# Optimization experiments

Measured on AMD Instinct MI355X. Metric: run time of the kernel, lower is better.

The kernel has to match this reference:

```python
import jax, jax.numpy as jnp
import numpy as np

B, S, D = 2, 2048, 1024
H, DH, DM = 16, 64, 4096
EPS = 1e-5
IGNORE = -100000.0


def setup_inputs() -> dict:
    key = jax.random.key(0)
    ks = jax.random.split(key, 14)
    s = 0.02
    return {
        "x": jax.random.normal(ks[0], (B, S, D), jnp.float32),
        "W_Q": jax.random.normal(ks[1], (H, DH, D), jnp.float32) * s,
        "W_K": jax.random.normal(ks[2], (H, DH, D), jnp.float32) * s,
        "W_V": jax.random.normal(ks[3], (H, DH, D), jnp.float32) * s,
        "W_O": jax.random.normal(ks[4], (H, D, DH), jnp.float32) * s,
        "b_Q": jax.random.normal(ks[5], (H, DH), jnp.float32) * s,
        "b_K": jax.random.normal(ks[6], (H, DH), jnp.float32) * s,
        "b_V": jax.random.normal(ks[7], (H, DH), jnp.float32) * s,
        "b_O": jax.random.normal(ks[8], (D,), jnp.float32) * s,
        "W_in": jax.random.normal(ks[9], (DM, D), jnp.float32) * s,
        "b_in": jax.random.normal(ks[10], (DM,), jnp.float32) * s,
        "W_out": jax.random.normal(ks[11], (D, DM), jnp.float32) * s,
        "b_out": jax.random.normal(ks[12], (D,), jnp.float32) * s,
    }


def ln_pre(x):
    x = x - jnp.mean(x, axis=-1, keepdims=True)
    scale = jnp.sqrt(jnp.mean(x * x, axis=-1, keepdims=True) + EPS)
    return x / scale


def gelu_new(x):
    c = np.sqrt(2.0 / np.pi).astype(np.float32)
    return 0.5 * x * (1.0 + jnp.tanh(c * (x + 0.044715 * x ** 3)))


def reference(x, W_Q, W_K, W_V, W_O, b_Q, b_K, b_V, b_O, W_in, b_in, W_out, b_out):
    resid_pre = x
    xn = ln_pre(resid_pre)
    # q,k,v: [B, S, H, DH]
    q = jnp.einsum('ihm,bpm->bpih', W_Q, xn) + b_Q
    k = jnp.einsum('ihm,bpm->bpih', W_K, xn) + b_K
    v = jnp.einsum('ihm,bpm->bpih', W_V, xn) + b_V
    attn_scale = np.sqrt(DH).astype(np.float32)
    # scores: [B, H, Sq, Sk]  (einsum 'bpih,bqih->bipq')
    scores = jnp.einsum('bpih,bqih->bipq', q, k) / attn_scale
    mask = jnp.tril(jnp.ones((S, S), bool))
    scores = jnp.where(mask, scores, IGNORE)
    attn = jax.nn.softmax(scores, axis=-1)
    # z: [B, Sq, H, DH]
    z = jnp.einsum('bpih,biqp->bqih', v, attn)
    attn_out = jnp.einsum('idh,bqih->bqd', W_O, z) + b_O
    resid_mid = resid_pre + attn_out
    m = ln_pre(resid_mid)
    pre = jnp.einsum('md,bpd->bpm', W_in, m) + b_in
    post = gelu_new(pre)
    mlp_out = jnp.einsum('dm,bpm->bpd', W_out, post) + b_out
    return resid_mid + mlp_out
```

## Files before the change

### kernel.cpp

```cpp
#include <hip/hip_runtime.h>

typedef unsigned short u16;
typedef __attribute__((ext_vector_type(8))) short short8;
typedef __attribute__((ext_vector_type(4))) unsigned short ushort4v;
typedef __attribute__((ext_vector_type(4))) float float4v;

__device__ __forceinline__ float bf2f(u16 u) {
  union { unsigned int i; float f; } c; c.i = ((unsigned int)u) << 16; return c.f;
}
__device__ __forceinline__ u16 f2bf(float f) {
  union { float f; unsigned int i; } c; c.f = f;
  unsigned int u = c.i;
  return (u16)((u + 0x7fffu + ((u >> 16) & 1u)) >> 16);
}
__device__ __forceinline__ unsigned int cvt_pk_bf16(float a, float b) {
  unsigned int r;
  asm("v_cvt_pk_bf16_f32 %0, %1, %2" : "=v"(r) : "v"(a), "v"(b));
  return r;
}
__device__ __forceinline__ float gelu_new(float x) {
  const float k1 = 2.30218776f;
  const float k3 = 0.10294233f;
  float x3 = x * x * x;
  float e = __builtin_amdgcn_exp2f(-(k1 * x + k3 * x3));
  return x / (1.0f + e);
}
__device__ __forceinline__ float ldres(const float* p) { return *p; }
__device__ __forceinline__ float ldres(const u16* p) { return bf2f(*p); }

__device__ __forceinline__ void gload_lds16(const u16* g, u16* l) {
  __builtin_amdgcn_global_load_lds(
      (const __attribute__((address_space(1))) unsigned int*)g,
      (__attribute__((address_space(3))) unsigned int*)l, 16, 0, 0);
}

__global__ void cvt_bf16_multi(const float* __restrict__ s0, const float* __restrict__ s1,
                               const float* __restrict__ s2, const float* __restrict__ s3,
                               const float* __restrict__ s4, u16* __restrict__ d0,
                               u16* __restrict__ d1, u16* __restrict__ d2,
                               u16* __restrict__ d3, u16* __restrict__ d4) {
  int bid = blockIdx.x;
  const float* src; u16* dst; int base;
  if (bid < 512)       { src = s0; dst = d0; base = 0; }
  else if (bid < 1024) { src = s1; dst = d1; base = 512; }
  else if (bid < 1536) { src = s2; dst = d2; base = 1024; }
  else if (bid < 3584) { src = s3; dst = d3; base = 1536; }
  else                 { src = s4; dst = d4; base = 3584; }
  int t = (bid - base) * 256 + threadIdx.x;
  float4v a = *(const float4v*)(src + (size_t)t * 8);
  float4v b = *(const float4v*)(src + (size_t)t * 8 + 4);
  short8 o;
#pragma unroll
  for (int j = 0; j < 4; ++j) o[j] = (short)f2bf(a[j]);
#pragma unroll
  for (int j = 0; j < 4; ++j) o[4 + j] = (short)f2bf(b[j]);
  *(short8*)(dst + (size_t)t * 8) = o;
}

__global__ void prep_wo(const float* __restrict__ WO, u16* __restrict__ Wot) {
  int t = blockIdx.x * 256 + threadIdx.x;
  int i = t >> 13;
  int d = (t >> 3) & 1023;
  int h0 = (t & 7) * 8;
  const float* src = WO + (size_t)i * 65536 + d * 64 + h0;
  float4v a = *(const float4v*)(src);
  float4v b = *(const float4v*)(src + 4);
  short8 o;
#pragma unroll
  for (int j = 0; j < 4; ++j) o[j] = (short)f2bf(a[j]);
#pragma unroll
  for (int j = 0; j < 4; ++j) o[4 + j] = (short)f2bf(b[j]);
  *(short8*)(Wot + (size_t)d * 1024 + i * 64 + h0) = o;
}

__global__ void prep_bqkv(const float* __restrict__ bQ, const float* __restrict__ bK,
                          const float* __restrict__ bV, float* __restrict__ bqkv) {
  int t = blockIdx.x * 256 + threadIdx.x;
  if (t < 3072)
    bqkv[t] = (t < 1024) ? bQ[t] : (t < 2048) ? bK[t - 1024] : bV[t - 2048];
}

__global__ void ln_f32(const float* __restrict__ x, u16* __restrict__ y) {
  __shared__ float red1[4];
  __shared__ float red2[4];
  int token = blockIdx.x;
  int tid = threadIdx.x;
  int w = tid >> 6;
  const float* xr = x + (size_t)token * 1024;
  float4v v = *(const float4v*)(xr + tid * 4);
  float s = v[0] + v[1] + v[2] + v[3];
#pragma unroll
  for (int m = 32; m >= 1; m >>= 1) s += __shfl_xor(s, m);
  if ((tid & 63) == 0) red1[w] = s;
  __syncthreads();
  float mean = (red1[0] + red1[1] + red1[2] + red1[3]) * (1.0f / 1024.0f);
  float ss = 0.0f;
#pragma unroll
  for (int j = 0; j < 4; ++j) { v[j] -= mean; ss += v[j] * v[j]; }
#pragma unroll
  for (int m = 32; m >= 1; m >>= 1) ss += __shfl_xor(ss, m);
  if ((tid & 63) == 0) red2[w] = ss;
  __syncthreads();
  float ms = (red2[0] + red2[1] + red2[2] + red2[3]) * (1.0f / 1024.0f);
  float inv = 1.0f / sqrtf(ms + 1e-5f);
  ushort4v o;
#pragma unroll
  for (int j = 0; j < 4; ++j) o[j] = f2bf(v[j] * inv);
  *(ushort4v*)(y + (size_t)token * 1024 + tid * 4) = o;
}

template <int BN, int BK, bool GELU, bool VSPLIT, bool DBUF, typename TO, typename TR>
__global__ __launch_bounds__(256) void gemm_bt(
    const u16* __restrict__ A, const u16* __restrict__ Bw,
    const float* __restrict__ bias, const TR* __restrict__ resid,
    TO* __restrict__ C, u16* __restrict__ vTout, int M, int N, int K,
    int lda, int ldc) {
  constexpr int BM = 128;
  constexpr int SEGS = BK / 8;
  constexpr int SMASK = SEGS - 1;
  constexpr int FI = 4, FJ = BN / 32;
  constexpr int CA = BM * SEGS / 256;
  constexpr int CB = BN * SEGS / 256;
  constexpr int NB = DBUF ? 2 : 1;
  __shared__ __align__(16) u16 As[NB][BM * BK];
  __shared__ __align__(16) u16 Bs[NB][BN * BK];
  const int tid = threadIdx.x;
  const int w = tid >> 6, lane = tid & 63;
  const int quad = lane >> 4, l16 = lane & 15;
  const int m0 = blockIdx.x * BM, n0 = blockIdx.y * BN;
  const int wm = (w >> 1) * 64, wn = (w & 1) * (BN / 2);
  const int rmask = l16 & SMASK;
  float4v acc[FI][FJ] = {};

  auto stage = [&](int buf, int k0) {
#pragma unroll
    for (int t = 0; t < CA; ++t) {
      int chunk = (w * CA + t) * 64 + lane;
      int row = chunk / SEGS, seg = chunk % SEGS;
      int sseg = seg ^ (row & SMASK);
      gload_lds16(A + (size_t)(m0 + row) * lda + k0 + sseg * 8,
                  As[buf] + (w * CA + t) * 512);
    }
#pragma unroll
    for (int t = 0; t < CB; ++t) {
      int chunk = (w * CB + t) * 64 + lane;
      int row = chunk / SEGS, seg = chunk % SEGS;
      int sseg = seg ^ (row & SMASK);
      gload_lds16(Bw + (size_t)(n0 + row) * K + k0 + sseg * 8,
                  Bs[buf] + (w * CB + t) * 512);
    }
  };
  auto compute = [&](int buf) {
#pragma unroll
    for (int kk = 0; kk < BK; kk += 32) {
      short8 a[FI], b[FJ];
#pragma unroll
      for (int fi = 0; fi < FI; ++fi)
        a[fi] = *(const short8*)(As[buf] + (wm + fi * 16 + l16) * BK +
                                 ((((kk >> 3) + quad) ^ rmask) << 3));
#pragma unroll
      for (int fj = 0; fj < FJ; ++fj)
        b[fj] = *(const short8*)(Bs[buf] + (wn + fj * 16 + l16) * BK +
                                 ((((kk >> 3) + quad) ^ rmask) << 3));
#pragma unroll
      for (int fi = 0; fi < FI; ++fi)
#pragma unroll
        for (int fj = 0; fj < FJ; ++fj)
          acc[fi][fj] = __builtin_amdgcn_mfma_f32_16x16x32_bf16(
              a[fi], b[fj], acc[fi][fj], 0, 0, 0);
    }
  };

  if constexpr (DBUF) {
    stage(0, 0);
    __syncthreads();
    int cur = 0;
    for (int k0 = 0; k0 < K; k0 += BK) {
      if (k0 + BK < K) stage(cur ^ 1, k0 + BK);
      compute(cur);
      __syncthreads();
      cur ^= 1;
    }
  } else {
    for (int k0 = 0; k0 < K; k0 += BK) {
      __syncthreads();
      stage(0, k0);
      __syncthreads();
      compute(0);
    }
  }

#pragma unroll
  for (int fi = 0; fi < FI; ++fi) {
#pragma unroll
    for (int fj = 0; fj < FJ; ++fj) {
      int col = n0 + wn + fj * 16 + l16;
      float bv = bias ? bias[col] : 0.0f;
#pragma unroll
      for (int r = 0; r < 4; ++r) {
        int row = m0 + wm + fi * 16 + quad * 4 + r;
        float val = acc[fi][fj][r] + bv;
        if (resid) val += ldres(resid + (size_t)row * N + col);
        if (GELU) val = gelu_new(val);
        if (VSPLIT && col < 1024) val *= 0.18033688011112042f;
        if (VSPLIT && col >= 2048) {
          vTout[(size_t)(col - 2048) * 4096 + row] = f2bf(val);
        } else if constexpr (sizeof(TO) == 2) {
          C[(size_t)row * ldc + col] = f2bf(val);
        } else {
          C[(size_t)row * ldc + col] = val;
        }
      }
    }
  }
}

__global__ __launch_bounds__(256) void attn_flash(u16* __restrict__ qk,
                                                  const u16* __restrict__ vT) {
  constexpr int PADK = 72;
  constexpr float THR2 = 10.0f;
  __shared__ __align__(16) u16 Ks[64 * PADK];
  __shared__ __align__(16) u16 Vt[64 * PADK];
  __shared__ __align__(16) u16 Ps[4][16 * PADK];
  const int id = blockIdx.x;
  const int qt = 31 - (id >> 5);
  const int combo = id & 31;
  const int head = combo >> 1, b = combo & 1;
  const int tid = threadIdx.x;
  const int w = tid >> 6, lane = tid & 63;
  const int quad = lane >> 4, l16 = lane & 15;
  const int q0 = qt * 64;
  const size_t tokB = (size_t)b * 2048;

  short8 aq[2];
#pragma unroll
  for (int ks = 0; ks < 2; ++ks)
    aq[ks] = *(const short8*)(qk + (tokB + q0 + w * 16 + l16) * 2048 +
                              head * 64 + ks * 32 + quad * 8);

  const u16* kbase = qk + tokB * 2048 + 1024 + head * 64;
  const u16* vbase = vT + (size_t)head * 64 * 4096 + tokB;

  short8 bones = {};
  if (l16 == 0) {
#pragma unroll
    for (int j = 0; j < 8; ++j) bones[j] = (short)0x3F80;
  }

  float m_st[4] = {-1e30f, -1e30f, -1e30f, -1e30f};
  float4v o_acc[4] = {};
  float4v o5 = {0.f, 0.f, 0.f, 0.f};

  const int srow = tid >> 2;
  const int sseg = (tid & 3) * 2;
  const u16* kptr = kbase + (size_t)srow * 2048 + sseg * 8;
  const u16* vptr = vbase + (size_t)srow * 4096 + sseg * 8;
  u16* ksl = Ks + srow * PADK + sseg * 8;
  u16* vsl = Vt + srow * PADK + sseg * 8;

  short8 pk0 = *(const short8*)(kptr);
  short8 pk1 = *(const short8*)(kptr + 8);
  short8 pv0 = *(const short8*)(vptr);
  short8 pv1 = *(const short8*)(vptr + 8);

  for (int kt = 0; kt <= qt; ++kt) {
    const int kk0 = kt * 64;
    __syncthreads();
    *(short8*)(ksl) = pk0;
    *(short8*)(ksl + 8) = pk1;
    *(short8*)(vsl) = pv0;
    *(short8*)(vsl + 8) = pv1;
    __syncthreads();
    if (kt < qt) {
      const u16* kp = kptr + (size_t)(kk0 + 64) * 2048;
      const u16* vp = vptr + kk0 + 64;
      pk0 = *(const short8*)(kp);
      pk1 = *(const short8*)(kp + 8);
      pv0 = *(const short8*)(vp);
      pv1 = *(const short8*)(vp + 8);
    }

    float4v s[4];
    __builtin_amdgcn_s_setprio(1);
#pragma unroll
    for (int fj = 0; fj < 4; ++fj) {
      float4v t = {0.f, 0.f, 0.f, 0.f};
#pragma unroll
      for (int ks = 0; ks < 2; ++ks) {
        short8 bk = *(const short8*)(Ks + (fj * 16 + l16) * PADK + ks * 32 + quad * 8);
        t = __builtin_amdgcn_mfma_f32_16x16x32_bf16(aq[ks], bk, t, 0, 0, 0);
      }
      s[fj] = t;
    }
    __builtin_amdgcn_s_setprio(0);
    if (kt == qt) {
#pragma unroll
      for (int fj = 0; fj < 4; ++fj) {
        int col = kk0 + fj * 16 + l16;
#pragma unroll
        for (int r = 0; r < 4; ++r) {
          int row = q0 + w * 16 + quad * 4 + r;
          if (col > row) s[fj][r] = -1e30f;
        }
      }
    }
    float mx[4];
#pragma unroll
    for (int r = 0; r < 4; ++r) {
      float m = fmaxf(fmaxf(s[0][r], s[1][r]), fmaxf(s[2][r], s[3][r]));
      m = fmaxf(m, __shfl_xor(m, 1));
      m = fmaxf(m, __shfl_xor(m, 2));
      m = fmaxf(m, __shfl_xor(m, 4));
      m = fmaxf(m, __shfl_xor(m, 8));
      mx[r] = m;
    }
    bool need = false;
#pragma unroll
    for (int r = 0; r < 4; ++r) need |= (mx[r] > m_st[r] + THR2);
    if (__any(need)) {
#pragma unroll
      for (int r = 0; r < 4; ++r) {
        float mnew = fmaxf(m_st[r], mx[r]);
        float al = __builtin_amdgcn_exp2f(m_st[r] - mnew);
        m_st[r] = mnew;
        o5[r] *= al;
#pragma unroll
        for (int fj = 0; fj < 4; ++fj) o_acc[fj][r] *= al;
      }
    }
#pragma unroll
    for (int fj = 0; fj < 4; ++fj) {
#pragma unroll
      for (int r = 0; r < 4; r += 2) {
        float e0 = __builtin_amdgcn_exp2f(s[fj][r] - m_st[r]);
        float e1 = __builtin_amdgcn_exp2f(s[fj][r + 1] - m_st[r + 1]);
        unsigned int pp = cvt_pk_bf16(e0, e1);
        Ps[w][(quad * 4 + r) * PADK + fj * 16 + l16] = (u16)pp;
        Ps[w][(quad * 4 + r + 1) * PADK + fj * 16 + l16] = (u16)(pp >> 16);
      }
    }
    short8 ap[2];
#pragma unroll
    for (int ks = 0; ks < 2; ++ks)
      ap[ks] = *(const short8*)(&Ps[w][l16 * PADK + ks * 32 + quad * 8]);
    __builtin_amdgcn_s_setprio(1);
#pragma unroll
    for (int fj = 0; fj < 4; ++fj)
#pragma unroll
      for (int ks = 0; ks < 2; ++ks) {
        short8 bv = *(const short8*)(Vt + (fj * 16 + l16) * PADK + ks * 32 + quad * 8);
        o_acc[fj] = __builtin_amdgcn_mfma_f32_16x16x32_bf16(ap[ks], bv, o_acc[fj], 0, 0, 0);
      }
#pragma unroll
    for (int ks = 0; ks < 2; ++ks)
      o5 = __builtin_amdgcn_mfma_f32_16x16x32_bf16(ap[ks], bones, o5, 0, 0, 0);
    __builtin_amdgcn_s_setprio(0);
  }
#pragma unroll
  for (int r = 0; r < 4; ++r) {
    float lsum = __shfl(o5[r], lane & 48);
    float inv = 1.0f / lsum;
    int row = q0 + w * 16 + quad * 4 + r;
#pragma unroll
    for (int fj = 0; fj < 4; ++fj)
      qk[(tokB + row) * 2048 + head * 64 + fj * 16 + l16] =
          f2bf(o_acc[fj][r] * inv);
  }
}

extern "C" void kernel_launch(void* const* d_in, const int* in_sizes, int n_in,
                              void* d_out, int out_size, void* d_ws, size_t ws_size,
                              hipStream_t stream) {
  const float* x = (const float*)d_in[0];
  const float* W_Q = (const float*)d_in[1];
  const float* W_K = (const float*)d_in[2];
  const float* W_V = (const float*)d_in[3];
  const float* W_O = (const float*)d_in[4];
  const float* b_Q = (const float*)d_in[5];
  const float* b_K = (const float*)d_in[6];
  const float* b_V = (const float*)d_in[7];
  const float* b_O = (const float*)d_in[8];
  const float* W_in = (const float*)d_in[9];
  const float* b_in = (const float*)d_in[10];
  const float* W_out = (const float*)d_in[11];
  const float* b_out = (const float*)d_in[12];
  float* out = (float*)d_out;

  char* ws = (char*)d_ws;
  u16* Wqkv = (u16*)(ws);
  u16* Wot  = (u16*)(ws + 6291456);
  u16* Wib  = (u16*)(ws + 8388608);
  u16* Wob  = (u16*)(ws + 16777216);
  float* bqkv = (float*)(ws + 25165824);
  u16* xn   = (u16*)(ws + 25178112);
  u16* qk   = (u16*)(ws + 33566720);
  u16* vT   = (u16*)(ws + 50343936);
  u16* hbuf = (u16*)(ws + 33566720);
  float* rm = (float*)(ws + 67121152);

  cvt_bf16_multi<<<5632, 256, 0, stream>>>(W_Q, W_K, W_V, W_in, W_out,
                                           Wqkv, Wqkv + 1048576, Wqkv + 2097152,
                                           Wib, Wob);
  prep_wo<<<512, 256, 0, stream>>>(W_O, Wot);
  prep_bqkv<<<12, 256, 0, stream>>>(b_Q, b_K, b_V, bqkv);

  ln_f32<<<4096, 256, 0, stream>>>(x, xn);
  gemm_bt<128, 64, false, true, false, u16, float><<<dim3(32, 24), 256, 0, stream>>>(
      xn, Wqkv, bqkv, (const float*)nullptr, qk, vT, 4096, 3072, 1024, 1024, 2048);
  attn_flash<<<1024, 256, 0, stream>>>(qk, vT);
  gemm_bt<64, 64, false, false, true, float, float><<<dim3(32, 16), 256, 0, stream>>>(
      qk , Wot, b_O, x, rm, nullptr, 4096, 1024, 1024, 2048, 1024);
  ln_f32<<<4096, 256, 0, stream>>>(rm, xn);
  gemm_bt<128, 64, true, false, false, u16, float><<<dim3(32, 32), 256, 0, stream>>>(
      xn, Wib, b_in, (const float*)nullptr, hbuf, nullptr, 4096, 4096, 1024, 1024, 4096);
  gemm_bt<64, 64, false, false, true, float, float><<<dim3(32, 16), 256, 0, stream>>>(
      hbuf, Wob, b_out, rm, out, nullptr, 4096, 1024, 4096, 4096, 1024);
}
```

Baseline: 366.5 us.

## Add 256x256-tile double-buffered GEMM kernel for MLP input projection

Introduces a new 512-thread GEMM kernel with 256x256 output tiles, XOR-swizzled LDS layout, two-stage direct-to-LDS prefetch pipelining, and XCD-aware block-to-tile mapping. It replaces the 128x64 tiled GEMM for the W_in projection with fused GELU. Larger tiles raise arithmetic intensity and cut redundant global loads. The trade-offs are 128KB of LDS per block, heavy register use (128 accumulator floats per thread), and only 256 blocks, which may limit occupancy and latency hiding.

```diff
diff --git a/kernel.cpp b/kernel.cpp
--- a/kernel.cpp
+++ b/kernel.cpp
@@ -215,6 +215,109 @@
   }
 }
 
+template <bool GELU>
+__global__ __launch_bounds__(512, 2) void gemm256(
+    const u16* __restrict__ A, const u16* __restrict__ Bw,
+    const float* __restrict__ bias, u16* __restrict__ C,
+    int M, int N, int K, int lda, int ldc) {
+  constexpr int BK = 64;
+  __shared__ __align__(16) u16 As[2][256 * BK];
+  __shared__ __align__(16) u16 Bs[2][256 * BK];
+  const int tid = threadIdx.x;
+  const int w = tid >> 6, lane = tid & 63;
+  const int quad = lane >> 4, l16 = lane & 15;
+  const int rmask = l16 & 7;
+  const int id = blockIdx.x;
+  const int xcd = id & 7, local = id >> 3;
+  const int mt = (xcd & 3) * 4 + (local >> 3);
+  const int ntile = (xcd >> 2) * 8 + (local & 7);
+  const int m0 = mt * 256, n0 = ntile * 256;
+  const int wm = (w >> 2) * 128, wn = (w & 3) * 64;
+
+  const u16* ag[4];
+  const u16* bg[4];
+#pragma unroll
+  for (int t = 0; t < 4; ++t) {
+    int chunk = (w * 4 + t) * 64 + lane;
+    int row = chunk >> 3, seg = chunk & 7;
+    int sseg = seg ^ (row & 7);
+    ag[t] = A + (size_t)(m0 + row) * lda + sseg * 8;
+    bg[t] = Bw + (size_t)(n0 + row) * K + sseg * 8;
+  }
+
+  float4v acc[8][4] = {};
+
+  auto stage = [&](int buf, int k0) {
+#pragma unroll
+    for (int t = 0; t < 4; ++t)
+      gload_lds16(ag[t] + k0, &As[buf][(w * 4 + t) * 512]);
+#pragma unroll
+    for (int t = 0; t < 4; ++t)
+      gload_lds16(bg[t] + k0, &Bs[buf][(w * 4 + t) * 512]);
+  };
+  auto compute = [&](int buf) {
+    const u16* Ab = &As[buf][0];
+    const u16* Bb = &Bs[buf][0];
+    short8 bfrag[4][2];
+#pragma unroll
+    for (int ni = 0; ni < 4; ++ni)
+#pragma unroll
+      for (int k2 = 0; k2 < 2; ++k2)
+        bfrag[ni][k2] = *(const short8*)(Bb + (wn + ni * 16 + l16) * BK +
+                                         (((k2 * 4 + quad) ^ rmask) << 3));
+#pragma unroll
+    for (int mi = 0; mi < 8; ++mi) {
+      short8 afrag[2];
+#pragma unroll
+      for (int k2 = 0; k2 < 2; ++k2)
+        afrag[k2] = *(const short8*)(Ab + (wm + mi * 16 + l16) * BK +
+                                     (((k2 * 4 + quad) ^ rmask) << 3));
+#pragma unroll
+      for (int ni = 0; ni < 4; ++ni)
+#pragma unroll
+        for (int k2 = 0; k2 < 2; ++k2)
+          acc[mi][ni] = __builtin_amdgcn_mfma_f32_16x16x32_bf16(
+              afrag[k2], bfrag[ni][k2], acc[mi][ni], 0, 0, 0);
+    }
+  };
+
+  const int ntk = K / BK;
+  stage(0, 0);
+  stage(1, BK);
+  asm volatile("s_waitcnt vmcnt(8)" ::: "memory");
+  asm volatile("s_barrier" ::: "memory");
+  int cur = 0;
+  for (int t = 0; t < ntk; ++t) {
+    compute(cur);
+    asm volatile("s_waitcnt lgkmcnt(0)" ::: "memory");
+    asm volatile("s_barrier" ::: "memory");
+    if (t + 2 < ntk) {
+      stage(cur, (t + 2) * BK);
+      asm volatile("s_waitcnt vmcnt(8)" ::: "memory");
+    } else {
+      asm volatile("s_waitcnt vmcnt(0)" ::: "memory");
+    }
+    asm volatile("s_barrier" ::: "memory");
+    cur ^= 1;
+  }
+
+#pragma unroll
+  for (int mi = 0; mi < 8; ++mi) {
+#pragma unroll
+    for (int ni = 0; ni < 4; ++ni) {
+      int col = n0 + wn + ni * 16 + l16;
+      float bv = bias[col];
+#pragma unroll
+      for (int r = 0; r < 4; ++r) {
+        int row = m0 + wm + mi * 16 + quad * 4 + r;
+        float val = acc[mi][ni][r] + bv;
+        if (GELU) val = gelu_new(val);
+        C[(size_t)row * ldc + col] = f2bf(val);
+      }
+    }
+  }
+}
+
 __global__ __launch_bounds__(256) void attn_flash(u16* __restrict__ qk,
                                                   const u16* __restrict__ vT) {
   constexpr int PADK = 72;
@@ -411,8 +514,8 @@
   gemm_bt<64, 64, false, false, true, float, float><<<dim3(32, 16), 256, 0, stream>>>(
       qk , Wot, b_O, x, rm, nullptr, 4096, 1024, 1024, 2048, 1024);
   ln_f32<<<4096, 256, 0, stream>>>(rm, xn);
-  gemm_bt<128, 64, true, false, false, u16, float><<<dim3(32, 32), 256, 0, stream>>>(
-      xn, Wib, b_in, (const float*)nullptr, hbuf, nullptr, 4096, 4096, 1024, 1024, 4096);
+  gemm256<true><<<256, 512, 0, stream>>>(xn, Wib, b_in, hbuf,
+                                         4096, 4096, 1024, 1024, 4096);
   gemm_bt<64, 64, false, false, true, float, float><<<dim3(32, 16), 256, 0, stream>>>(
       hbuf, Wob, b_out, rm, out, nullptr, 4096, 1024, 4096, 4096, 1024);
 }
```

Result: faster. 354.7 us (-3.2%).

## Use 256x256-tile pipelined GEMM kernel for the MLP input projection

Applied to the files above, without the earlier changes.

Adds a gemm256 kernel with 512 threads per block, 256x256 output tiles, double-buffered direct global-to-LDS loads, swizzled LDS layout, interleaved load/MFMA phases with barriers, and XCD-aware tile mapping. It replaces the 128x64 generic GEMM used for W_in plus GELU. The aim is more data reuse per tile and overlap of loads with MFMA. In exchange it uses heavy register and LDS pressure and launches only 256 blocks.

```diff
diff --git a/kernel.cpp b/kernel.cpp
--- a/kernel.cpp
+++ b/kernel.cpp
@@ -215,6 +215,133 @@
   }
 }
 
+template <bool GELU>
+__global__ __launch_bounds__(512, 2) void gemm256(
+    const u16* __restrict__ A, const u16* __restrict__ Bw,
+    const float* __restrict__ bias, u16* __restrict__ C,
+    int M, int N, int K, int lda, int ldc) {
+  __shared__ __align__(16) u16 As[2][2][128 * 64];
+  __shared__ __align__(16) u16 Bs[2][2][128 * 64];
+  const int tid = threadIdx.x;
+  const int w = tid >> 6, lane = tid & 63;
+  const int quad = lane >> 4, l16 = lane & 15;
+  const int rmask = l16 & 7;
+  const int id = blockIdx.x;
+  const int xcd = id & 7, local = id >> 3;
+  const int mt = (xcd & 3) * 4 + (local >> 3);
+  const int nt = (xcd >> 2) * 8 + (local & 7);
+  const int m0 = mt * 256, n0 = nt * 256;
+  const int aHalf = w >> 2;
+  const int bHalf = (w & 3) >> 1;
+  const int bRow0 = (w & 1) * 64;
+
+  const int srow = lane >> 3, sq = lane & 7;
+  int row_[2], ss_[2];
+#pragma unroll
+  for (int i = 0; i < 2; ++i) {
+    row_[i] = (w * 2 + i) * 8 + srow;
+    ss_[i] = sq ^ (row_[i] & 7);
+  }
+  const u16* aSrc[2][2];
+  const u16* bSrc[2][2];
+#pragma unroll
+  for (int i = 0; i < 2; ++i)
+#pragma unroll
+    for (int hf = 0; hf < 2; ++hf) {
+      aSrc[i][hf] = A + (size_t)(m0 + hf * 128 + row_[i]) * lda + ss_[i] * 8;
+      bSrc[i][hf] = Bw + (size_t)(n0 + hf * 128 + row_[i]) * K + ss_[i] * 8;
+    }
+
+  const int ntk = K >> 6;
+  const int nIt = ntk >> 1;
+
+  float4v acc[8][4] = {};
+  short8 af[4][2], bf[2][2];
+
+  auto dsA = [&](int buf, int mh) {
+#pragma unroll
+    for (int mi = 0; mi < 4; ++mi)
+#pragma unroll
+      for (int k2 = 0; k2 < 2; ++k2)
+        af[mi][k2] = *(const short8*)(&As[buf][aHalf][(mh * 64 + mi * 16 + l16) * 64 +
+                                                      (((k2 * 4 + quad) ^ rmask) << 3)]);
+  };
+  auto dsB = [&](int buf, int nh) {
+#pragma unroll
+    for (int nb = 0; nb < 2; ++nb)
+#pragma unroll
+      for (int k2 = 0; k2 < 2; ++k2)
+        bf[nb][k2] = *(const short8*)(&Bs[buf][bHalf][(bRow0 + (nh * 2 + nb) * 16 + l16) * 64 +
+                                                      (((k2 * 4 + quad) ^ rmask) << 3)]);
+  };
+  auto mfmaQ = [&](int mh, int nh) {
+    __builtin_amdgcn_s_setprio(1);
+#pragma unroll
+    for (int mi = 0; mi < 4; ++mi)
+#pragma unroll
+      for (int nb = 0; nb < 2; ++nb)
+#pragma unroll
+        for (int k2 = 0; k2 < 2; ++k2)
+          acc[mh * 4 + mi][nh * 2 + nb] = __builtin_amdgcn_mfma_f32_16x16x32_bf16(
+              af[mi][k2], bf[nb][k2], acc[mh * 4 + mi][nh * 2 + nb], 0, 0, 0);
+    __builtin_amdgcn_s_setprio(0);
+  };
+  auto stA = [&](int t, int hf) {
+    if (t < ntk) {
+#pragma unroll
+      for (int i = 0; i < 2; ++i)
+        gload_lds16(aSrc[i][hf] + t * 64, &As[t & 1][hf][(w * 2 + i) * 512]);
+    }
+  };
+  auto stB = [&](int t, int hf) {
+    if (t < ntk) {
+#pragma unroll
+      for (int i = 0; i < 2; ++i)
+        gload_lds16(bSrc[i][hf] + t * 64, &Bs[t & 1][hf][(w * 2 + i) * 512]);
+    }
+  };
+#define BAR() asm volatile("s_barrier" ::: "memory")
+
+  stA(0, 0); stA(0, 1); stB(0, 0); stB(0, 1); stA(1, 0);
+  asm volatile("s_waitcnt vmcnt(2)" ::: "memory");
+  BAR();
+
+  for (int j = 0; j < nIt; ++j) {
+    const int T1 = 2 * j + 1, T2 = 2 * j + 2, T3 = 2 * j + 3;
+    const bool last = (j == nIt - 1);
+    dsA(0, 0); dsB(0, 0); stA(T1, 1); BAR(); mfmaQ(0, 0); BAR();
+    dsB(0, 1);            stB(T1, 0); BAR(); mfmaQ(0, 1); BAR();
+    dsA(0, 1);            stB(T1, 1); BAR(); mfmaQ(1, 1); BAR();
+    dsB(0, 0);            stA(T2, 0);
+    if (last) { asm volatile("s_waitcnt vmcnt(0)" ::: "memory"); }
+    else      { asm volatile("s_waitcnt vmcnt(2)" ::: "memory"); }
+    BAR(); mfmaQ(1, 0); BAR();
+    dsA(1, 0); dsB(1, 0); stA(T2, 1); BAR(); mfmaQ(0, 0); BAR();
+    dsB(1, 1);            stB(T2, 0); BAR(); mfmaQ(0, 1); BAR();
+    dsA(1, 1);            stB(T2, 1); BAR(); mfmaQ(1, 1); BAR();
+    dsB(1, 0);            stA(T3, 0);
+    if (!last) { asm volatile("s_waitcnt vmcnt(2)" ::: "memory"); }
+    BAR(); mfmaQ(1, 0); BAR();
+  }
+#undef BAR
+
+#pragma unroll
+  for (int mi = 0; mi < 8; ++mi) {
+#pragma unroll
+    for (int ni = 0; ni < 4; ++ni) {
+      int col = n0 + (w & 3) * 64 + ni * 16 + l16;
+      float bv = bias[col];
+#pragma unroll
+      for (int r = 0; r < 4; ++r) {
+        int row = m0 + (w >> 2) * 128 + mi * 16 + quad * 4 + r;
+        float val = acc[mi][ni][r] + bv;
+        if (GELU) val = gelu_new(val);
+        C[(size_t)row * ldc + col] = f2bf(val);
+      }
+    }
+  }
+}
+
 __global__ __launch_bounds__(256) void attn_flash(u16* __restrict__ qk,
                                                   const u16* __restrict__ vT) {
   constexpr int PADK = 72;
@@ -411,8 +538,8 @@
   gemm_bt<64, 64, false, false, true, float, float><<<dim3(32, 16), 256, 0, stream>>>(
       qk , Wot, b_O, x, rm, nullptr, 4096, 1024, 1024, 2048, 1024);
   ln_f32<<<4096, 256, 0, stream>>>(rm, xn);
-  gemm_bt<128, 64, true, false, false, u16, float><<<dim3(32, 32), 256, 0, stream>>>(
-      xn, Wib, b_in, (const float*)nullptr, hbuf, nullptr, 4096, 4096, 1024, 1024, 4096);
+  gemm256<true><<<256, 512, 0, stream>>>(xn, Wib, b_in, hbuf,
+                                         4096, 4096, 1024, 1024, 4096);
   gemm_bt<64, 64, false, false, true, float, float><<<dim3(32, 16), 256, 0, stream>>>(
       hbuf, Wob, b_out, rm, out, nullptr, 4096, 1024, 4096, 4096, 1024);
 }
```

Result: faster. 355.6 us (-3.0%).
